# Optimization experiments

Hardware: AMD Instinct MI355X
Metric: run time of the kernel (lower is better)

## Reference

```python
import jax, jax.numpy as jnp
import numpy as np

LN_EPS = 1e-6  # flax.linen.LayerNorm default

def _layernorm(x, scale, bias):
    mu = jnp.mean(x, axis=-1, keepdims=True)
    var = jnp.mean(jnp.square(x - mu), axis=-1, keepdims=True)
    return (x - mu) * jax.lax.rsqrt(var + LN_EPS) * scale + bias

def setup_inputs() -> dict:
    key = jax.random.key(0)
    ks = jax.random.split(key, 16)
    N, D = 65536, 512
    W = 1024  # hidden width for all 4 layers
    def init_w(k, fan_in, fan_out):
        # lecun_normal (flax Dense default kernel init)
        return jax.random.normal(k, (fan_in, fan_out), jnp.float32) / np.sqrt(fan_in)
    return {
        "descriptors": jax.random.normal(ks[0], (N, D), jnp.float32),
        "W0": init_w(ks[1], D, W),
        "b0": jnp.zeros((W,), jnp.float32),
        "W1": init_w(ks[2], W, W),
        "g1": jnp.ones((W,), jnp.float32),
        "be1": jnp.zeros((W,), jnp.float32),
        "W2": init_w(ks[3], W, W),
        "g2": jnp.ones((W,), jnp.float32),
        "be2": jnp.zeros((W,), jnp.float32),
        "W3": init_w(ks[4], W, W),
        "g3": jnp.ones((W,), jnp.float32),
        "be3": jnp.zeros((W,), jnp.float32),
        "Wout": init_w(ks[5], W, 1),
        "bout": jnp.zeros((1,), jnp.float32),
    }

def reference(descriptors, W0, b0, W1, g1, be1, W2, g2, be2, W3, g3, be3, Wout, bout):
    # layer 0: Dense (with bias) -> relu
    h = jax.nn.relu(descriptors @ W0 + b0)  # [N, 1024]
    # hidden layers: bias-free Dense -> LayerNorm -> relu
    for Wk, gk, bk in ((W1, g1, be1), (W2, g2, be2), (W3, g3, be3)):
        h = jax.nn.relu(_layernorm(h @ Wk, gk, bk))
    # output: Dense(1) with bias -> relu
    return jax.nn.relu(h @ Wout + bout)  # [N, 1]
```

## Files before the change

kernel.cpp:

```cpp
#include <hip/hip_runtime.h>

typedef _Float16 f16;
typedef _Float16 f16x8 __attribute__((ext_vector_type(8)));
typedef float f32x16 __attribute__((ext_vector_type(16)));

#define TM 128
#define TN 256
#define BK 64

__device__ __forceinline__ void async_cp16(const void* g, void* l) {
  __builtin_amdgcn_global_load_lds(
      (const __attribute__((address_space(1))) void*)g,
      (__attribute__((address_space(3))) void*)l, 16, 0, 0);
}

template <int EPI>
__global__ __launch_bounds__(256, 2) void gemm_f16(
    const f16* __restrict__ A, const f16* __restrict__ Bt,
    const float* __restrict__ bias, f16* __restrict__ C,
    int M, int N, int K) {
  __shared__ alignas(16) f16 sA[TM][BK];
  __shared__ alignas(16) f16 sB[TN][BK];
  const int tid = threadIdx.x;
  const int lane = tid & 63;
  const int wave = tid >> 6;

  int mt, nt;
  if (gridDim.x == 4 && gridDim.y == 512) {
    const int id = blockIdx.y * 4 + blockIdx.x;
    nt = (id >> 3) & 3;
    mt = (id & 7) * 64 + (id >> 5);
  } else {
    nt = blockIdx.x;
    mt = blockIdx.y;
  }
  const long long bm = (long long)mt * TM;
  const long long bn = (long long)nt * TN;

  const int wm = (wave & 1) * 64;
  const int wn = (wave >> 1) * 128;
  const int l31 = lane & 31;
  const int half = lane >> 5;

  const f16* const Abase = A + bm * (long long)K;
  const f16* const Bbase = Bt + bn * (long long)K;
  int aOff[4], bOff[8];
#pragma unroll
  for (int i = 0; i < 4; ++i) {
    const int chunk = wave * 256 + i * 64 + lane;
    const int ml = chunk >> 3;
    const int kc = (chunk & 7) ^ (ml & 7);
    aOff[i] = ml * K + kc * 8;
  }
#pragma unroll
  for (int i = 0; i < 8; ++i) {
    const int chunk = wave * 512 + i * 64 + lane;
    const int ml = chunk >> 3;
    const int kc = (chunk & 7) ^ (ml & 7);
    bOff[i] = ml * K + kc * 8;
  }

  f32x16 acc[2][4] = {};

  const int kIters = K / BK;
  for (int kt = 0; kt < kIters; ++kt) {
    const int k0 = kt * BK;
#pragma unroll
    for (int i = 0; i < 4; ++i)
      async_cp16(Abase + aOff[i] + k0,
                 &sA[0][0] + (wave * 256 + i * 64) * 8);
#pragma unroll
    for (int i = 0; i < 8; ++i)
      async_cp16(Bbase + bOff[i] + k0,
                 &sB[0][0] + (wave * 512 + i * 64) * 8);
    __syncthreads();

#pragma unroll
    for (int s = 0; s < 4; ++s) {
      const int csw = ((s * 2 + half) ^ (lane & 7)) * 8;
      f16x8 af[2], bf[4];
#pragma unroll
      for (int i = 0; i < 2; ++i) af[i] = *(const f16x8*)&sA[wm + i * 32 + l31][csw];
#pragma unroll
      for (int j = 0; j < 4; ++j) bf[j] = *(const f16x8*)&sB[wn + j * 32 + l31][csw];
#pragma unroll
      for (int i = 0; i < 2; ++i)
#pragma unroll
        for (int j = 0; j < 4; ++j)
          acc[i][j] = __builtin_amdgcn_mfma_f32_32x32x16_f16(af[i], bf[j],
                                                             acc[i][j], 0, 0, 0);
    }
    __syncthreads();
  }

#pragma unroll
  for (int i = 0; i < 2; ++i)
#pragma unroll
    for (int j = 0; j < 4; ++j) {
      const long long colg = bn + wn + j * 32 + l31;
      float bval = 0.f;
      if (EPI == 0) bval = bias[colg];
#pragma unroll
      for (int reg = 0; reg < 16; ++reg) {
        const long long rowg =
            bm + wm + i * 32 + (reg & 3) + 8 * (reg >> 2) + 4 * half;
        float v = acc[i][j][reg];
        if (EPI == 0) v = fmaxf(v + bval, 0.f);
        C[rowg * N + colg] = (f16)v;
      }
    }
}

__global__ __launch_bounds__(256) void ln_relu_kernel(
    const f16* __restrict__ Y, const float* __restrict__ g,
    const float* __restrict__ b, f16* __restrict__ H) {
  const int lane = threadIdx.x & 63;
  const int wave = threadIdx.x >> 6;
  const long long row = (long long)blockIdx.x * 4 + wave;
  const f16* y = Y + row * 1024;
  float x[16];
  float s1 = 0.f, s2 = 0.f;
#pragma unroll
  for (int p = 0; p < 2; ++p) {
    f16x8 v = *(const f16x8*)(y + p * 512 + lane * 8);
#pragma unroll
    for (int e = 0; e < 8; ++e) {
      const float f = (float)v[e];
      x[p * 8 + e] = f;
      s1 += f;
      s2 += f * f;
    }
  }
#pragma unroll
  for (int off = 32; off >= 1; off >>= 1) {
    s1 += __shfl_xor(s1, off);
    s2 += __shfl_xor(s2, off);
  }
  const float mean = s1 * (1.f / 1024.f);
  const float var = fmaxf(s2 * (1.f / 1024.f) - mean * mean, 0.f);
  const float inv = rsqrtf(var + 1e-6f);
  f16* h = H + row * 1024;
#pragma unroll
  for (int p = 0; p < 2; ++p) {
    f16x8 o;
#pragma unroll
    for (int e = 0; e < 8; ++e) {
      const int c = p * 512 + lane * 8 + e;
      const float v = (x[p * 8 + e] - mean) * inv * g[c] + b[c];
      o[e] = (f16)fmaxf(v, 0.f);
    }
    *(f16x8*)(h + p * 512 + lane * 8) = o;
  }
}

__global__ __launch_bounds__(256) void ln_relu_out_kernel(
    const f16* __restrict__ Y, const float* __restrict__ g,
    const float* __restrict__ b, const float* __restrict__ Wout,
    const float* __restrict__ bout, float* __restrict__ out) {
  const int lane = threadIdx.x & 63;
  const int wave = threadIdx.x >> 6;
  const long long row = (long long)blockIdx.x * 4 + wave;
  const f16* y = Y + row * 1024;
  float x[16];
  float s1 = 0.f, s2 = 0.f;
#pragma unroll
  for (int p = 0; p < 2; ++p) {
    f16x8 v = *(const f16x8*)(y + p * 512 + lane * 8);
#pragma unroll
    for (int e = 0; e < 8; ++e) {
      const float f = (float)v[e];
      x[p * 8 + e] = f;
      s1 += f;
      s2 += f * f;
    }
  }
#pragma unroll
  for (int off = 32; off >= 1; off >>= 1) {
    s1 += __shfl_xor(s1, off);
    s2 += __shfl_xor(s2, off);
  }
  const float mean = s1 * (1.f / 1024.f);
  const float var = fmaxf(s2 * (1.f / 1024.f) - mean * mean, 0.f);
  const float inv = rsqrtf(var + 1e-6f);
  float dot = 0.f;
#pragma unroll
  for (int p = 0; p < 2; ++p) {
#pragma unroll
    for (int e = 0; e < 8; ++e) {
      const int c = p * 512 + lane * 8 + e;
      const float v = fmaxf((x[p * 8 + e] - mean) * inv * g[c] + b[c], 0.f);
      dot += v * Wout[c];
    }
  }
#pragma unroll
  for (int off = 32; off >= 1; off >>= 1) dot += __shfl_xor(dot, off);
  if (lane == 0) out[row] = fmaxf(dot + bout[0], 0.f);
}

__global__ __launch_bounds__(256) void cvt_f16_kernel(const float* __restrict__ X,
                                                      f16* __restrict__ Y,
                                                      long long n) {
  const long long i = ((long long)blockIdx.x * 256 + threadIdx.x) * 8;
  if (i >= n) return;
  const float4* X4 = (const float4*)(X + i);
  const float4 a = X4[0], c = X4[1];
  f16x8 o;
  o[0] = (f16)a.x; o[1] = (f16)a.y; o[2] = (f16)a.z; o[3] = (f16)a.w;
  o[4] = (f16)c.x; o[5] = (f16)c.y; o[6] = (f16)c.z; o[7] = (f16)c.w;
  *(f16x8*)(Y + i) = o;
}

__global__ __launch_bounds__(256) void transpose_cvt(const float* __restrict__ W,
                                                     f16* __restrict__ Wt, int K,
                                                     int N) {
  __shared__ float tile[64][65];
  const int bn = blockIdx.x * 64;
  const int bk = blockIdx.y * 64;
  const int tx = threadIdx.x & 63;
  const int ty = threadIdx.x >> 6;
#pragma unroll
  for (int i = 0; i < 64; i += 4)
    tile[ty + i][tx] = W[(long long)(bk + ty + i) * N + bn + tx];
  __syncthreads();
#pragma unroll
  for (int i = 0; i < 64; i += 4)
    Wt[(long long)(bn + ty + i) * K + bk + tx] = (f16)tile[tx][ty + i];
}

extern "C" void kernel_launch(void* const* d_in, const int* in_sizes, int n_in,
                              void* d_out, int out_size, void* d_ws, size_t ws_size,
                              hipStream_t stream) {
  const float* desc = (const float*)d_in[0];
  const float* W0 = (const float*)d_in[1];
  const float* b0 = (const float*)d_in[2];
  const float* W1 = (const float*)d_in[3];
  const float* g1 = (const float*)d_in[4];
  const float* be1 = (const float*)d_in[5];
  const float* W2 = (const float*)d_in[6];
  const float* g2 = (const float*)d_in[7];
  const float* be2 = (const float*)d_in[8];
  const float* W3 = (const float*)d_in[9];
  const float* g3 = (const float*)d_in[10];
  const float* be3 = (const float*)d_in[11];
  const float* Wout = (const float*)d_in[12];
  const float* bout = (const float*)d_in[13];
  float* out = (float*)d_out;

  const long long Nrows = 65536, D = 512, W = 1024;
  char* p = (char*)d_ws;
  f16* descH = (f16*)p; p += Nrows * D * sizeof(f16);
  f16* Wt0 = (f16*)p;   p += D * W * sizeof(f16);
  f16* Wt1 = (f16*)p;   p += W * W * sizeof(f16);
  f16* Wt2 = (f16*)p;   p += W * W * sizeof(f16);
  f16* Wt3 = (f16*)p;   p += W * W * sizeof(f16);
  f16* H = (f16*)p;     p += Nrows * W * sizeof(f16);
  f16* Y = (f16*)p;     p += Nrows * W * sizeof(f16);
  (void)ws_size; (void)in_sizes; (void)n_in; (void)out_size;

  cvt_f16_kernel<<<(int)(Nrows * D / 8 / 256), 256, 0, stream>>>(desc, descH,
                                                                 Nrows * D);
  transpose_cvt<<<dim3(W / 64, D / 64), 256, 0, stream>>>(W0, Wt0, (int)D, (int)W);
  transpose_cvt<<<dim3(W / 64, W / 64), 256, 0, stream>>>(W1, Wt1, (int)W, (int)W);
  transpose_cvt<<<dim3(W / 64, W / 64), 256, 0, stream>>>(W2, Wt2, (int)W, (int)W);
  transpose_cvt<<<dim3(W / 64, W / 64), 256, 0, stream>>>(W3, Wt3, (int)W, (int)W);

  dim3 ggrid(W / TN, Nrows / TM);
  gemm_f16<0><<<ggrid, 256, 0, stream>>>(descH, Wt0, b0, H, (int)Nrows, (int)W, (int)D);

  gemm_f16<1><<<ggrid, 256, 0, stream>>>(H, Wt1, nullptr, Y, (int)Nrows, (int)W, (int)W);
  ln_relu_kernel<<<(int)(Nrows / 4), 256, 0, stream>>>(Y, g1, be1, H);

  gemm_f16<1><<<ggrid, 256, 0, stream>>>(H, Wt2, nullptr, Y, (int)Nrows, (int)W, (int)W);
  ln_relu_kernel<<<(int)(Nrows / 4), 256, 0, stream>>>(Y, g2, be2, H);

  gemm_f16<1><<<ggrid, 256, 0, stream>>>(H, Wt3, nullptr, Y, (int)Nrows, (int)W, (int)W);
  ln_relu_out_kernel<<<(int)(Nrows / 4), 256, 0, stream>>>(Y, g3, be3, Wout, bout, out);
}
```

Before: 888.0 us.

## Fuse LayerNorm stats into GEMM epilogue and normalization into next GEMM prologue

The GEMMs for layers 1 and 2 now accumulate per-row sum and sum-of-squares with atomics in their epilogue. The following GEMM applies LayerNorm, scale, bias and ReLU in f16 while loading its A tile, so the two standalone ln_relu passes over the activations are removed. This saves two full read/write sweeps of the 128MB activation buffer. In exchange the A operand is loaded synchronously through registers instead of async global-to-LDS copies, the normalization runs in f16, and contended atomics are added to the epilogue.

```diff
diff --git a/kernel.cpp b/kernel.cpp
--- a/kernel.cpp
+++ b/kernel.cpp
@@ -14,11 +14,12 @@
       (__attribute__((address_space(3))) void*)l, 16, 0, 0);
 }
 
-template <int EPI>
+template <int AMODE, int EPI, int STATS>
 __global__ __launch_bounds__(256, 2) void gemm_f16(
     const f16* __restrict__ A, const f16* __restrict__ Bt,
-    const float* __restrict__ bias, f16* __restrict__ C,
-    int M, int N, int K) {
+    const float* __restrict__ bias, const float2* __restrict__ stats_in,
+    const f16* __restrict__ gh, const f16* __restrict__ beh,
+    float* __restrict__ stats_out, f16* __restrict__ C, int M, int N, int K) {
   __shared__ alignas(16) f16 sA[TM][BK];
   __shared__ alignas(16) f16 sB[TN][BK];
   const int tid = threadIdx.x;
@@ -44,13 +45,12 @@
 
   const f16* const Abase = A + bm * (long long)K;
   const f16* const Bbase = Bt + bn * (long long)K;
+  const int aKc = (lane & 7) ^ ((wave * 32 + (lane >> 3)) & 7);
   int aOff[4], bOff[8];
 #pragma unroll
   for (int i = 0; i < 4; ++i) {
-    const int chunk = wave * 256 + i * 64 + lane;
-    const int ml = chunk >> 3;
-    const int kc = (chunk & 7) ^ (ml & 7);
-    aOff[i] = ml * K + kc * 8;
+    const int ml = wave * 32 + i * 8 + (lane >> 3);
+    aOff[i] = ml * K + aKc * 8;
   }
 #pragma unroll
   for (int i = 0; i < 8; ++i) {
@@ -60,19 +60,45 @@
     bOff[i] = ml * K + kc * 8;
   }
 
+  f16 rstdh[4], nmrh[4];
+  if (AMODE == 1) {
+#pragma unroll
+    for (int i = 0; i < 4; ++i) {
+      const int ml = wave * 32 + i * 8 + (lane >> 3);
+      const float2 sv = stats_in[bm + ml];
+      const float mean = sv.x * (1.f / 1024.f);
+      const float var = fmaxf(sv.y * (1.f / 1024.f) - mean * mean, 0.f);
+      const float rs = rsqrtf(var + 1e-6f);
+      rstdh[i] = (f16)rs;
+      nmrh[i] = (f16)(-mean * rs);
+    }
+  }
+
   f32x16 acc[2][4] = {};
 
   const int kIters = K / BK;
   for (int kt = 0; kt < kIters; ++kt) {
     const int k0 = kt * BK;
-#pragma unroll
-    for (int i = 0; i < 4; ++i)
-      async_cp16(Abase + aOff[i] + k0,
-                 &sA[0][0] + (wave * 256 + i * 64) * 8);
+    if (AMODE == 0) {
+#pragma unroll
+      for (int i = 0; i < 4; ++i)
+        async_cp16(Abase + aOff[i] + k0, &sA[0][0] + (wave * 256 + i * 64) * 8);
+    } else {
+      const f16x8 g8 = *(const f16x8*)(gh + k0 + aKc * 8);
+      const f16x8 be8 = *(const f16x8*)(beh + k0 + aKc * 8);
+#pragma unroll
+      for (int i = 0; i < 4; ++i) {
+        f16x8 y = *(const f16x8*)(Abase + aOff[i] + k0);
+        f16x8 t = y * rstdh[i] + nmrh[i];
+        f16x8 o = t * g8 + be8;
+#pragma unroll
+        for (int e = 0; e < 8; ++e) o[e] = o[e] > (f16)0.f ? o[e] : (f16)0.f;
+        *(f16x8*)(&sA[0][0] + (wave * 256 + i * 64 + lane) * 8) = o;
+      }
+    }
 #pragma unroll
     for (int i = 0; i < 8; ++i)
-      async_cp16(Bbase + bOff[i] + k0,
-                 &sB[0][0] + (wave * 512 + i * 64) * 8);
+      async_cp16(Bbase + bOff[i] + k0, &sB[0][0] + (wave * 512 + i * 64) * 8);
     __syncthreads();
 
 #pragma unroll
@@ -93,63 +119,49 @@
     __syncthreads();
   }
 
-#pragma unroll
-  for (int i = 0; i < 2; ++i)
-#pragma unroll
-    for (int j = 0; j < 4; ++j) {
-      const long long colg = bn + wn + j * 32 + l31;
-      float bval = 0.f;
-      if (EPI == 0) bval = bias[colg];
+  if (STATS) {
+#pragma unroll
+    for (int i = 0; i < 2; ++i)
 #pragma unroll
       for (int reg = 0; reg < 16; ++reg) {
         const long long rowg =
             bm + wm + i * 32 + (reg & 3) + 8 * (reg >> 2) + 4 * half;
-        float v = acc[i][j][reg];
-        if (EPI == 0) v = fmaxf(v + bval, 0.f);
-        C[rowg * N + colg] = (f16)v;
+        float e1 = 0.f, e2 = 0.f;
+#pragma unroll
+        for (int j = 0; j < 4; ++j) {
+          const long long colg = bn + wn + j * 32 + l31;
+          const float v = acc[i][j][reg];
+          C[rowg * N + colg] = (f16)v;
+          e1 += v;
+          e2 += v * v;
+        }
+#pragma unroll
+        for (int off = 16; off >= 1; off >>= 1) {
+          e1 += __shfl_xor(e1, off);
+          e2 += __shfl_xor(e2, off);
+        }
+        if (l31 == 0) {
+          atomicAdd(&stats_out[2 * rowg], e1);
+          atomicAdd(&stats_out[2 * rowg + 1], e2);
+        }
       }
-    }
-}
-
-__global__ __launch_bounds__(256) void ln_relu_kernel(
-    const f16* __restrict__ Y, const float* __restrict__ g,
-    const float* __restrict__ b, f16* __restrict__ H) {
-  const int lane = threadIdx.x & 63;
-  const int wave = threadIdx.x >> 6;
-  const long long row = (long long)blockIdx.x * 4 + wave;
-  const f16* y = Y + row * 1024;
-  float x[16];
-  float s1 = 0.f, s2 = 0.f;
-#pragma unroll
-  for (int p = 0; p < 2; ++p) {
-    f16x8 v = *(const f16x8*)(y + p * 512 + lane * 8);
-#pragma unroll
-    for (int e = 0; e < 8; ++e) {
-      const float f = (float)v[e];
-      x[p * 8 + e] = f;
-      s1 += f;
-      s2 += f * f;
-    }
-  }
-#pragma unroll
-  for (int off = 32; off >= 1; off >>= 1) {
-    s1 += __shfl_xor(s1, off);
-    s2 += __shfl_xor(s2, off);
-  }
-  const float mean = s1 * (1.f / 1024.f);
-  const float var = fmaxf(s2 * (1.f / 1024.f) - mean * mean, 0.f);
-  const float inv = rsqrtf(var + 1e-6f);
-  f16* h = H + row * 1024;
-#pragma unroll
-  for (int p = 0; p < 2; ++p) {
-    f16x8 o;
-#pragma unroll
-    for (int e = 0; e < 8; ++e) {
-      const int c = p * 512 + lane * 8 + e;
-      const float v = (x[p * 8 + e] - mean) * inv * g[c] + b[c];
-      o[e] = (f16)fmaxf(v, 0.f);
-    }
-    *(f16x8*)(h + p * 512 + lane * 8) = o;
+  } else {
+#pragma unroll
+    for (int i = 0; i < 2; ++i)
+#pragma unroll
+      for (int j = 0; j < 4; ++j) {
+        const long long colg = bn + wn + j * 32 + l31;
+        float bval = 0.f;
+        if (EPI == 0) bval = bias[colg];
+#pragma unroll
+        for (int reg = 0; reg < 16; ++reg) {
+          const long long rowg =
+              bm + wm + i * 32 + (reg & 3) + 8 * (reg >> 2) + 4 * half;
+          float v = acc[i][j][reg];
+          if (EPI == 0) v = fmaxf(v + bval, 0.f);
+          C[rowg * N + colg] = (f16)v;
+        }
+      }
   }
 }
 
@@ -195,6 +207,12 @@
 #pragma unroll
   for (int off = 32; off >= 1; off >>= 1) dot += __shfl_xor(dot, off);
   if (lane == 0) out[row] = fmaxf(dot + bout[0], 0.f);
+}
+
+__global__ __launch_bounds__(256) void zero_f32_kernel(float* __restrict__ p,
+                                                       int n) {
+  const int i = (blockIdx.x * 256 + threadIdx.x) * 4;
+  if (i < n) *(float4*)(p + i) = float4{0.f, 0.f, 0.f, 0.f};
 }
 
 __global__ __launch_bounds__(256) void cvt_f16_kernel(const float* __restrict__ X,
@@ -208,6 +226,18 @@
   o[0] = (f16)a.x; o[1] = (f16)a.y; o[2] = (f16)a.z; o[3] = (f16)a.w;
   o[4] = (f16)c.x; o[5] = (f16)c.y; o[6] = (f16)c.z; o[7] = (f16)c.w;
   *(f16x8*)(Y + i) = o;
+}
+
+__global__ void cvt_gb_kernel(const float* __restrict__ g1,
+                              const float* __restrict__ be1,
+                              const float* __restrict__ g2,
+                              const float* __restrict__ be2,
+                              f16* __restrict__ o) {
+  const int t = threadIdx.x;
+  o[t] = (f16)g1[t];
+  o[1024 + t] = (f16)be1[t];
+  o[2048 + t] = (f16)g2[t];
+  o[3072 + t] = (f16)be2[t];
 }
 
 __global__ __launch_bounds__(256) void transpose_cvt(const float* __restrict__ W,
@@ -255,8 +285,13 @@
   f16* Wt3 = (f16*)p;   p += W * W * sizeof(f16);
   f16* H = (f16*)p;     p += Nrows * W * sizeof(f16);
   f16* Y = (f16*)p;     p += Nrows * W * sizeof(f16);
+  float* S1 = (float*)p; p += Nrows * 2 * sizeof(float);
+  float* S2 = (float*)p; p += Nrows * 2 * sizeof(float);
+  f16* ghb = (f16*)p;   p += 4096 * sizeof(f16);
   (void)ws_size; (void)in_sizes; (void)n_in; (void)out_size;
 
+  zero_f32_kernel<<<(int)(Nrows * 4 / 4 / 256), 256, 0, stream>>>(S1, (int)(Nrows * 4));
+  cvt_gb_kernel<<<1, 1024, 0, stream>>>(g1, be1, g2, be2, ghb);
   cvt_f16_kernel<<<(int)(Nrows * D / 8 / 256), 256, 0, stream>>>(desc, descH,
                                                                  Nrows * D);
   transpose_cvt<<<dim3(W / 64, D / 64), 256, 0, stream>>>(W0, Wt0, (int)D, (int)W);
@@ -265,14 +300,18 @@
   transpose_cvt<<<dim3(W / 64, W / 64), 256, 0, stream>>>(W3, Wt3, (int)W, (int)W);
 
   dim3 ggrid(W / TN, Nrows / TM);
-  gemm_f16<0><<<ggrid, 256, 0, stream>>>(descH, Wt0, b0, H, (int)Nrows, (int)W, (int)D);
-
-  gemm_f16<1><<<ggrid, 256, 0, stream>>>(H, Wt1, nullptr, Y, (int)Nrows, (int)W, (int)W);
-  ln_relu_kernel<<<(int)(Nrows / 4), 256, 0, stream>>>(Y, g1, be1, H);
-
-  gemm_f16<1><<<ggrid, 256, 0, stream>>>(H, Wt2, nullptr, Y, (int)Nrows, (int)W, (int)W);
-  ln_relu_kernel<<<(int)(Nrows / 4), 256, 0, stream>>>(Y, g2, be2, H);
-
-  gemm_f16<1><<<ggrid, 256, 0, stream>>>(H, Wt3, nullptr, Y, (int)Nrows, (int)W, (int)W);
-  ln_relu_out_kernel<<<(int)(Nrows / 4), 256, 0, stream>>>(Y, g3, be3, Wout, bout, out);
-}
+  gemm_f16<0, 0, 0><<<ggrid, 256, 0, stream>>>(descH, Wt0, b0, nullptr, nullptr,
+                                               nullptr, nullptr, H, (int)Nrows,
+                                               (int)W, (int)D);
+  gemm_f16<0, 1, 1><<<ggrid, 256, 0, stream>>>(H, Wt1, nullptr, nullptr, nullptr,
+                                               nullptr, S1, Y, (int)Nrows, (int)W,
+                                               (int)W);
+  gemm_f16<1, 1, 1><<<ggrid, 256, 0, stream>>>(Y, Wt2, nullptr, (const float2*)S1,
+                                               ghb, ghb + 1024, S2, H, (int)Nrows,
+                                               (int)W, (int)W);
+  gemm_f16<1, 1, 0><<<ggrid, 256, 0, stream>>>(H, Wt3, nullptr, (const float2*)S2,
+                                               ghb + 2048, ghb + 3072, nullptr, Y,
+                                               (int)Nrows, (int)W, (int)W);
+  ln_relu_out_kernel<<<(int)(Nrows / 4), 256, 0, stream>>>(Y, g3, be3, Wout, bout,
+                                                           out);
+}
```

Result: slower. 995.3 us (+12.1%).
